# Optimization experiments

Measured on AMD Instinct MI355X. Metric: run time of the kernel, lower is better.

Reference implementation:

```python
import jax, jax.numpy as jnp
import numpy as np

B, T, IDIM, HDIM, K, LMAX, NLAYERS = 64, 1024, 120, 320, 72, 96, 3
LAMB = 0.1
NEG = -1e30


def lse3(a, b, c):
    m = jnp.maximum(jnp.maximum(a, b), c)
    return m + jnp.log(jnp.exp(a - m) + jnp.exp(b - m) + jnp.exp(c - m))


def _lstm_dir(x, Wih, Whh, bb):
    # x: [B,T,D] -> h: [B,T,H]; PyTorch gate order i,f,g,o
    gx = jnp.einsum('btd,gd->tbg', x, Wih) + bb  # [T,B,4H]
    def step(carry, g):
        h, c = carry
        g = g + h @ Whh.T
        i, f, gg, o = jnp.split(g, 4, axis=-1)
        c = jax.nn.sigmoid(f) * c + jax.nn.sigmoid(i) * jnp.tanh(gg)
        h = jax.nn.sigmoid(o) * jnp.tanh(c)
        return (h, c), h
    h0 = jnp.zeros((x.shape[0], HDIM), x.dtype)
    _, hs = jax.lax.scan(step, (h0, h0), gx)
    return hs.transpose(1, 0, 2)


def _rev(x, lengths):
    # reverse each sequence within its valid length (packed-sequence semantics)
    t = jnp.arange(x.shape[1])
    idx = jnp.where(t[None, :] < lengths[:, None], lengths[:, None] - 1 - t[None, :], t[None, :])
    return jnp.take_along_axis(x, idx[:, :, None], axis=1)


def _blstm_layer(x, Wih_f, Whh_f, b_f, Wih_b, Whh_b, b_b, lengths):
    hf = _lstm_dir(x, Wih_f, Whh_f, b_f)
    hb = _rev(_lstm_dir(_rev(x, lengths), Wih_b, Whh_b, b_b), lengths)
    return jnp.concatenate([hf, hb], axis=2)


def _ctc_forward(logp, labels, in_lens, lab_lens):
    # standard CTC alpha recursion (blank=0), log-space, vectorized over batch
    Bn, Tn, _ = logp.shape
    S = 2 * LMAX + 1
    ext = jnp.zeros((Bn, S), jnp.int32).at[:, 1::2].set(labels)  # blank-interleaved labels
    em = jnp.take_along_axis(logp, jnp.broadcast_to(ext[:, None, :], (Bn, Tn, S)), axis=2)
    em = em.transpose(1, 0, 2)  # [T,B,S]
    s_idx = jnp.arange(S)
    prev_lab = jnp.concatenate([jnp.full((Bn, 2), -1, jnp.int32), ext[:, :-2]], axis=1)
    can_skip = ((s_idx[None, :] % 2) == 1) & (ext != prev_lab)
    valid_s = s_idx[None, :] < (2 * lab_lens[:, None] + 1)
    alpha0 = jnp.full((Bn, S), NEG, logp.dtype)
    alpha0 = alpha0.at[:, 0].set(em[0][:, 0]).at[:, 1].set(em[0][:, 1])
    alpha0 = jnp.where(valid_s, alpha0, NEG)
    def step(alpha, inp):
        em_t, t = inp
        a2 = jnp.concatenate([jnp.full((Bn, 1), NEG, alpha.dtype), alpha[:, :-1]], axis=1)
        a3 = jnp.concatenate([jnp.full((Bn, 2), NEG, alpha.dtype), alpha[:, :-2]], axis=1)
        a3 = jnp.where(can_skip, a3, NEG)
        new = lse3(alpha, a2, a3) + em_t
        new = jnp.where(valid_s, new, NEG)
        new = jnp.where((t < in_lens)[:, None], new, alpha)  # freeze past utterance end
        return new, None
    alpha, _ = jax.lax.scan(step, alpha0, (em[1:], jnp.arange(1, Tn)))
    last = 2 * lab_lens
    aL = jnp.take_along_axis(alpha, last[:, None], axis=1)[:, 0]
    aLm1 = jnp.take_along_axis(alpha, (last - 1)[:, None], axis=1)[:, 0]
    return jnp.logaddexp(aL, aLm1)  # log p(labels | x)


def setup_inputs():
    key = jax.random.key(0)
    ks = jax.random.split(key, 12)
    H4 = 4 * HDIM
    s = 0.05
    return dict(
        logits=jax.random.normal(ks[0], (B, T, IDIM), jnp.float32),
        labels_padded=jax.random.randint(ks[1], (B, LMAX), 1, K).astype(jnp.int32),
        input_lengths=jax.random.randint(ks[2], (B,), T // 2, T + 1).astype(jnp.int32),
        label_lengths=jax.random.randint(ks[3], (B,), LMAX // 2, LMAX + 1).astype(jnp.int32),
        Wih0=jax.random.normal(ks[4], (2, H4, IDIM), jnp.float32) * s,
        Whh0=jax.random.normal(ks[5], (2, H4, HDIM), jnp.float32) * s,
        b0=jnp.zeros((2, H4), jnp.float32),
        Wih=jax.random.normal(ks[6], (NLAYERS - 1, 2, H4, 2 * HDIM), jnp.float32) * s,
        Whh=jax.random.normal(ks[7], (NLAYERS - 1, 2, H4, HDIM), jnp.float32) * s,
        b=jnp.zeros((NLAYERS - 1, 2, H4), jnp.float32),
        W_lin=jax.random.normal(ks[8], (K, 2 * HDIM), jnp.float32) * s,
        b_lin=jnp.zeros((K,), jnp.float32),
    )


def reference(logits, labels_padded, input_lengths, label_lengths, Wih0, Whh0, b0, Wih, Whh, b, W_lin, b_lin):
    # sort by input length descending (mirrors torch.sort + index_select)
    order = jnp.argsort(-input_lengths)
    logits = logits[order]
    labels_padded = labels_padded[order]
    input_lengths = input_lengths[order]
    label_lengths = label_lengths[order]
    # 3-layer BLSTM encoder
    x = _blstm_layer(logits, Wih0[0], Whh0[0], b0[0], Wih0[1], Whh0[1], b0[1], input_lengths)
    for l in range(NLAYERS - 1):
        x = _blstm_layer(x, Wih[l, 0], Whh[l, 0], b[l, 0], Wih[l, 1], Whh[l, 1], b[l, 1], input_lengths)
    netout = jax.nn.log_softmax(x @ W_lin.T + b_lin, axis=2)  # [B,T,K]
    # CTC-CRF: numerator = CTC alpha log-prob; denominator = free-running partition
    num = _ctc_forward(netout, labels_padded, input_lengths, label_lengths)
    tmask = jnp.arange(netout.shape[1])[None, :] < input_lengths[:, None]
    den = jnp.sum(jnp.where(tmask, jax.nn.logsumexp(netout, axis=2), 0.0), axis=1)
    return jnp.mean(den - (1.0 + LAMB) * num)
```

## Files before the change

### kernel.cpp

```cpp
#include <hip/hip_runtime.h>
#include <cstdint>
#include <cstddef>


typedef _Float16 f16;
typedef _Float16 h2v   __attribute__((ext_vector_type(2)));
typedef _Float16 f16x4v __attribute__((ext_vector_type(4)));
typedef _Float16 f16x8 __attribute__((ext_vector_type(8)));
typedef float    f32x4 __attribute__((ext_vector_type(4)));
typedef uint32_t u32x4 __attribute__((ext_vector_type(4)));

#define NEGF (-1e30f)
#define CT 128

__device__ __forceinline__ float dot2f(h2v a, h2v b, float c) {
#if __has_builtin(__builtin_amdgcn_fdot2)
  return __builtin_amdgcn_fdot2(a, b, c, false);
#else
  return c + (float)a.x * (float)b.x + (float)a.y * (float)b.y;
#endif
}

__device__ __forceinline__ float fast_rcp(float x) {
#if __has_builtin(__builtin_amdgcn_rcpf)
  return __builtin_amdgcn_rcpf(x);
#else
  return 1.f / x;
#endif
}
__device__ __forceinline__ float fsigm(float x) { return fast_rcp(1.f + __expf(-x)); }
__device__ __forceinline__ float ftanh(float x) { return 1.f - 2.f * fast_rcp(1.f + __expf(2.f * x)); }

__device__ __forceinline__ float fexp2(float x) {
#if __has_builtin(__builtin_amdgcn_exp2f)
  return __builtin_amdgcn_exp2f(x);
#else
  return exp2f(x);
#endif
}
__device__ __forceinline__ float flog2(float x) {
#if __has_builtin(__builtin_amdgcn_logf)
  return __builtin_amdgcn_logf(x);
#else
  return log2f(x);
#endif
}

__device__ __forceinline__ uint32_t poll_l2(const uint32_t* p) {
  uint32_t v;
  asm volatile("global_load_dword %0, %1, off sc0\n\t"
               "s_waitcnt vmcnt(0)"
               : "=&v"(v)
               : "v"(p)
               : "memory");
  return v;
}

__device__ __forceinline__ void stage16(f16* lds, const f16* g) {
#if __has_builtin(__builtin_amdgcn_global_load_lds)
  __builtin_amdgcn_global_load_lds(
      (const __attribute__((address_space(1))) uint32_t*)g,
      (__attribute__((address_space(3))) uint32_t*)lds, 16, 0, 0);
#else
  int lane = threadIdx.x & 63;
  *(f16x8*)&lds[lane * 8] = *(const f16x8*)g;
#endif
}


__global__ void conv_logits(const float* __restrict__ src, f16* __restrict__ dst) {
  int idx = blockIdx.x * 256 + threadIdx.x;
  int row = idx >> 7, k = idx & 127;
  dst[idx] = (f16)((k < 120) ? src[(size_t)row * 120 + k] : 0.f);
}

__global__ void conv_wt0(const float* __restrict__ w, f16* __restrict__ dst) {
  int idx = blockIdx.x * 256 + threadIdx.x;
  int n = idx >> 7, k = idx & 127;
  dst[idx] = (f16)((k < 120) ? w[(size_t)n * 120 + k] : 0.f);
}

__global__ void conv_copy(const float* __restrict__ src, f16* __restrict__ dst, int count) {
  int idx = blockIdx.x * 256 + threadIdx.x;
  if (idx < count) dst[idx] = (f16)src[idx];
}

__global__ void conv_wtl(const float* __restrict__ w, f16* __restrict__ dst) {
  int idx = blockIdx.x * 256 + threadIdx.x;
  int n = idx / 640, k = idx % 640;
  dst[idx] = (f16)((n < 72) ? w[(size_t)n * 640 + k] : 0.f);
}

__global__ void conv_whh(const float* __restrict__ whh0, const float* __restrict__ whh,
                         uint32_t* __restrict__ dst) {
  int o = blockIdx.x * 256 + threadIdx.x;
  int tid = o & 511;
  int g  = o >> 9;
  int j  = g % 40;
  int g2 = g / 40;
  int i  = g2 % 5;
  int g3 = g2 / 5;
  int hf = g3 & 1, slot = g3 >> 1;
  int tau = i * 512 + tid;
  int lr = tau >> 2, kq = tau & 3;
  int gate = lr / 160, u = lr - gate * 160;
  int r = gate * 320 + hf * 160 + u;
  int k = kq * 80 + j * 2;
  const float* srcm = (slot < 2) ? (whh0 + ((size_t)slot * 1280 + r) * 320)
                                 : (whh  + ((size_t)(slot - 2) * 1280 + r) * 320);
  f16 lo = (f16)srcm[k], hi = (f16)srcm[k + 1];
  dst[o] = (uint32_t)__builtin_bit_cast(unsigned short, lo) |
           ((uint32_t)__builtin_bit_cast(unsigned short, hi) << 16);
}

__global__ __launch_bounds__(256)
void gemm_chunk(const f16* __restrict__ A, const f16* __restrict__ W,
                f16* __restrict__ gxc, const int* __restrict__ lens,
                int lda, int kTiles, int c0) {
  __shared__ __align__(16) f16 As[128 * 32];
  __shared__ __align__(16) f16 Ws[2][128 * 32];
  const int tid = threadIdx.x;
  const int lane = tid & 63, wid = tid >> 6;
  const int wm = wid >> 1, wn = wid & 1;
  const int dir = blockIdx.y >> 6, b = blockIdx.y & 63;
  const int n0 = blockIdx.x * 256;
  const int r_base = lane >> 2;
  const int chs = ((((lane & 3) + (r_base >> 1)) & 3)) * 8;
  const int len = lens[b];

  f32x4 acc[4][8] = {};

  for (int kt = 0; kt < kTiles; ++kt) {
    const int k0 = kt * 32;
    __syncthreads();
#pragma unroll
    for (int hh = 0; hh < 2; ++hh) {
      const int c = wid * 2 + hh;
      const int j = c * 16 + r_base;
      const int s = c0 * CT + j;
      const int tt = dir ? ((s < len) ? (len - 1 - s) : s) : s;
      stage16(&As[c * 512], A + (size_t)(b * 1024 + tt) * lda + k0 + chs);
    }
#pragma unroll
    for (int hh = 0; hh < 4; ++hh) {
      const int c = wid * 4 + hh;
      const int tile = c >> 3, cc = c & 7;
      stage16(&Ws[tile][cc * 512],
              W + (size_t)(dir * 1280 + n0 + tile * 128 + cc * 16 + r_base) * lda + k0 + chs);
    }
    __syncthreads();

    const int q = lane >> 4;
    const int l15 = lane & 15;
    const int cs = (q - (l15 >> 1)) & 3;
    const int rofs = l15 * 32 + cs * 8;
    f16x8 av[4], wv0[4], wv1[4];
#pragma unroll
    for (int i = 0; i < 4; ++i)
      av[i] = *(const f16x8*)&As[(wm * 4 + i) * 512 + rofs];
#pragma unroll
    for (int i = 0; i < 4; ++i) {
      wv0[i] = *(const f16x8*)&Ws[0][(wn * 4 + i) * 512 + rofs];
      wv1[i] = *(const f16x8*)&Ws[1][(wn * 4 + i) * 512 + rofs];
    }
#pragma unroll
    for (int i = 0; i < 4; ++i)
#pragma unroll
      for (int j = 0; j < 4; ++j) {
        acc[i][j]     = __builtin_amdgcn_mfma_f32_16x16x32_f16(av[i], wv0[j], acc[i][j], 0, 0, 0);
        acc[i][4 + j] = __builtin_amdgcn_mfma_f32_16x16x32_f16(av[i], wv1[j], acc[i][4 + j], 0, 0, 0);
      }
  }

  const int r0 = (lane >> 4) * 4, cn = lane & 15;
  const size_t obase = (size_t)(dir * 64 + b) * CT;
#pragma unroll
  for (int i = 0; i < 4; ++i) {
    const int m = wm * 64 + i * 16 + r0;
#pragma unroll
    for (int j = 0; j < 4; ++j) {
      const int n = n0 + wn * 64 + j * 16 + cn;
#pragma unroll
      for (int r = 0; r < 4; ++r) {
        gxc[(obase + m + r) * 1280 + n]       = (f16)acc[i][j][r];
        gxc[(obase + m + r) * 1280 + n + 128] = (f16)acc[i][4 + j][r];
      }
    }
  }
}

__global__ void __launch_bounds__(512)
__attribute__((amdgpu_waves_per_eu(2, 2)))
lstm_scan_chunk(const volatile uint32_t* wbuf,
                const f16* __restrict__ gxc,
                const float* __restrict__ bias,
                const int* __restrict__ lens,
                f16* xnext,
                uint32_t* xq,
                uint32_t* xqf,
                f16* hsave,
                float* csave,
                int layer, int c0) {
  const int wg = blockIdx.x;
  const int half = wg >> 7;
  const int bd = wg & 127;
  const int b = bd >> 1, dir = bd & 1;
  const int tid = threadIdx.x;

  __shared__ __align__(16) f16 hbuf[320];
  __shared__ float ylds[640];
  __shared__ __align__(16) f16 hstage[64 * 160];

  h2v w[5][40];
  {
    const volatile uint32_t* wb =
        wbuf + (size_t)((layer * 2 + dir) * 2 + half) * 200 * 512;
#pragma unroll
    for (int i = 0; i < 5; ++i)
#pragma unroll
      for (int j = 0; j < 40; ++j) {
        uint32_t v = wb[(i * 40 + j) * 512 + tid];
        w[i][j] = __builtin_bit_cast(h2v, v);
      }
  }
  if (tid < 320) hbuf[tid] = (c0 == 0) ? (f16)0.f : hsave[bd * 320 + tid];

  const int len = lens[b];
  const int kq = tid & 3;
  const int qi = tid >> 2;
  const int gu = half * 160 + tid;
  float c_state = 0.f;
  float bi = 0.f, bff = 0.f, bg = 0.f, bo = 0.f;
  if (tid < 160) {
    if (c0 > 0) c_state = csave[wg * 160 + tid];
    const float* bp = bias + dir * 1280 + gu;
    bi = bp[0]; bff = bp[320]; bg = bp[640]; bo = bp[960];
  }
  __syncthreads();

  const size_t grow0 = (size_t)(dir * 64 + b) * CT;

  float gxi = 0.f, gxf = 0.f, gxg = 0.f, gxo = 0.f;
  if (tid < 160) {
    const f16* gp = gxc + grow0 * 1280 + gu;
    gxi = (float)gp[0]; gxf = (float)gp[320]; gxg = (float)gp[640]; gxo = (float)gp[960];
  }

  int fastmiss = 0;

  for (int tl = 0; tl < CT; ++tl) {
    const int s = c0 * CT + tl;
    const uint32_t tag = (uint32_t)(layer * 1024 + s + 1);

    float nxi = 0.f, nxf = 0.f, nxg = 0.f, nxo = 0.f;
    if (tid < 160 && tl + 1 < CT) {
      const f16* gp = gxc + (grow0 + tl + 1) * 1280 + gu;
      nxi = (float)gp[0]; nxf = (float)gp[320]; nxg = (float)gp[640]; nxo = (float)gp[960];
    }

    float a0 = 0.f, a1 = 0.f, a2 = 0.f, a3 = 0.f, a4 = 0.f;
    {
      const u32x4* h4 = (const u32x4*)hbuf;
#pragma unroll
      for (int jb = 0; jb < 5; ++jb) {
        u32x4 p = h4[kq * 10 + jb * 2];
        u32x4 q = h4[kq * 10 + jb * 2 + 1];
        h2v hr[8];
#pragma unroll
        for (int j = 0; j < 4; ++j) hr[j] = __builtin_bit_cast(h2v, p[j]);
#pragma unroll
        for (int j = 0; j < 4; ++j) hr[4 + j] = __builtin_bit_cast(h2v, q[j]);
#pragma unroll
        for (int j = 0; j < 8; ++j) {
          a0 = dot2f(w[0][jb * 8 + j], hr[j], a0);
          a1 = dot2f(w[1][jb * 8 + j], hr[j], a1);
          a2 = dot2f(w[2][jb * 8 + j], hr[j], a2);
          a3 = dot2f(w[3][jb * 8 + j], hr[j], a3);
          a4 = dot2f(w[4][jb * 8 + j], hr[j], a4);
        }
      }
    }
    {
      float av[5] = {a0, a1, a2, a3, a4};
#pragma unroll
      for (int i = 0; i < 5; ++i) {
        float v = av[i];
        v += __shfl_xor(v, 1, 64);
        v += __shfl_xor(v, 2, 64);
        if (kq == 0) ylds[i * 128 + qi] = v;
      }
    }

    if ((tl & 31) == 0 && tl > 0) {
      const int tw = tl - 32;
#pragma unroll
      for (int it = 0; it < 2; ++it) {
        const int slot = it * 512 + tid;
        if (slot < 640) {
          const int r = (int)(((unsigned)slot * 52429u) >> 20);
          const int j = slot - r * 20;
          const int sp = c0 * CT + tw + r;
          const int ttp = dir ? ((sp < len) ? (len - 1 - sp) : sp) : sp;
          f16x8 v = *(const f16x8*)&hstage[((tw + r) & 63) * 160 + j * 8];
          *(f16x8*)&xnext[(size_t)(b * 1024 + ttp) * 640 + dir * 320 + half * 160 + j * 8] = v;
        }
      }
    }
    __syncthreads();

    if (tid < 160) {
      const int u = tid;
      float pi = ylds[u]       + gxi + bi;
      float pf = ylds[160 + u] + gxf + bff;
      float pg = ylds[320 + u] + gxg + bg;
      float po = ylds[480 + u] + gxo + bo;
      float ig = fsigm(pi);
      float fg = fsigm(pf);
      float gg = ftanh(pg);
      float og = fsigm(po);
      c_state = fg * c_state + ig * gg;
      float hv = og * ftanh(c_state);
      const f16 hh = (f16)hv;
      const uint32_t word = (tag << 16) |
                            (uint32_t)__builtin_bit_cast(unsigned short, hh);
      const int qidx = ((bd * 2 + half) * 2 + (s & 1)) * 160 + u;
      __hip_atomic_store(&xqf[qidx], word, __ATOMIC_RELAXED,
                         __HIP_MEMORY_SCOPE_WORKGROUP);
      __hip_atomic_store(&xq[qidx], word, __ATOMIC_RELAXED,
                         __HIP_MEMORY_SCOPE_AGENT);
      hbuf[gu] = hh;
      hstage[(tl & 63) * 160 + u] = hh;
    } else if (tid >= 256 && tid < 416) {
      const int u = tid - 256;
      const int qidx = ((bd * 2 + (1 - half)) * 2 + (s & 1)) * 160 + u;
      uint32_t pw = 0;
      bool got = false;
      if (fastmiss < 2) {
        int tries = 16;
        do {
          pw = poll_l2(&xqf[qidx]);
        } while ((pw >> 16) != tag && --tries);
        got = ((pw >> 16) == tag);
        fastmiss = got ? 0 : (fastmiss + 1);
      }
      if (!got) {
        int spins = 0;
        do {
          pw = __hip_atomic_load(&xq[qidx], __ATOMIC_RELAXED,
                                 __HIP_MEMORY_SCOPE_AGENT);
        } while ((pw >> 16) != tag && ++spins < 200000);
      }
      hbuf[(1 - half) * 160 + u] =
          __builtin_bit_cast(f16, (unsigned short)(pw & 0xffffu));
    }
    __syncthreads();

    gxi = nxi; gxf = nxf; gxg = nxg; gxo = nxo;
  }

  {
    const int tw = CT - 32;
#pragma unroll
    for (int it = 0; it < 2; ++it) {
      const int slot = it * 512 + tid;
      if (slot < 640) {
        const int r = (int)(((unsigned)slot * 52429u) >> 20);
        const int j = slot - r * 20;
        const int sp = c0 * CT + tw + r;
        const int ttp = dir ? ((sp < len) ? (len - 1 - sp) : sp) : sp;
        f16x8 v = *(const f16x8*)&hstage[((tw + r) & 63) * 160 + j * 8];
        *(f16x8*)&xnext[(size_t)(b * 1024 + ttp) * 640 + dir * 320 + half * 160 + j * 8] = v;
      }
    }
  }
  if (tid < 160) {
    hsave[bd * 320 + gu] = hbuf[gu];
    csave[wg * 160 + tid] = c_state;
  }
}

__global__ __launch_bounds__(256)
void gemm_proj(const f16* __restrict__ A, const f16* __restrict__ W,
               float* __restrict__ outf, int lda, int kTiles, int ldo) {
  __shared__ __align__(16) f16 As[128 * 32];
  __shared__ __align__(16) f16 Ws[128 * 32];
  const int tid = threadIdx.x;
  const int lane = tid & 63, wid = tid >> 6;
  const int wm = wid >> 1, wn = wid & 1;
  const int m0 = blockIdx.y * 128, n0 = blockIdx.x * 128;
  const int r_base = lane >> 2;
  const int chs = ((((lane & 3) + (r_base >> 1)) & 3)) * 8;

  f32x4 acc[4][4] = {};

  for (int kt = 0; kt < kTiles; ++kt) {
    const int k0 = kt * 32;
    __syncthreads();
#pragma unroll
    for (int hh = 0; hh < 2; ++hh) {
      const int c = wid * 2 + hh;
      stage16(&As[c * 512], A + (size_t)(m0 + c * 16 + r_base) * lda + k0 + chs);
      stage16(&Ws[c * 512], W + (size_t)(n0 + c * 16 + r_base) * lda + k0 + chs);
    }
    __syncthreads();

    const int q = lane >> 4;
    const int l15 = lane & 15;
    const int cs = (q - (l15 >> 1)) & 3;
    const int rofs = l15 * 32 + cs * 8;
    f16x8 av[4], wv[4];
#pragma unroll
    for (int i = 0; i < 4; ++i)
      av[i] = *(const f16x8*)&As[(wm * 4 + i) * 512 + rofs];
#pragma unroll
    for (int i = 0; i < 4; ++i)
      wv[i] = *(const f16x8*)&Ws[(wn * 4 + i) * 512 + rofs];
#pragma unroll
    for (int i = 0; i < 4; ++i)
#pragma unroll
      for (int j = 0; j < 4; ++j)
        acc[i][j] = __builtin_amdgcn_mfma_f32_16x16x32_f16(av[i], wv[j], acc[i][j], 0, 0, 0);
  }

  const int r0 = (lane >> 4) * 4, cn = lane & 15;
#pragma unroll
  for (int i = 0; i < 4; ++i) {
    const int m = m0 + wm * 64 + i * 16 + r0;
#pragma unroll
    for (int j = 0; j < 4; ++j) {
      const int n = n0 + wn * 64 + j * 16 + cn;
#pragma unroll
      for (int r = 0; r < 4; ++r)
        outf[(size_t)(m + r) * ldo + n] = acc[i][j][r];
    }
  }
}

__global__ void lse_kernel(const float* __restrict__ Z, const float* __restrict__ b_lin,
                           float* __restrict__ lseout) {
  int row = blockIdx.x * 4 + (threadIdx.x >> 6);
  int l = threadIdx.x & 63;
  const float* z = Z + (size_t)row * 128;
  float v0 = (l < 72) ? z[l] + b_lin[l] : NEGF;
  float v1 = (l < 8) ? z[l + 64] + b_lin[l + 64] : NEGF;
  float m = fmaxf(v0, v1);
#pragma unroll
  for (int o = 32; o; o >>= 1) m = fmaxf(m, __shfl_xor(m, o, 64));
  float s = ((l < 72) ? __expf(v0 - m) : 0.f) + ((l < 8) ? __expf(v1 - m) : 0.f);
#pragma unroll
  for (int o = 32; o; o >>= 1) s += __shfl_xor(s, o, 64);
  if (l == 0) lseout[row] = m + __logf(s);
}

__global__ void emz_kernel(const float* __restrict__ Z, const float* __restrict__ lse,
                           const float* __restrict__ b_lin,
                           const int* __restrict__ labels,
                           f16* __restrict__ emc) {
  const int b = blockIdx.y;
  const int t0 = blockIdx.x * 4;
  const int tid = threadIdx.x;
  __shared__ int ext[200];
  __shared__ float bls[200];
  if (tid < 200) {
    int e = (tid < 193 && (tid & 1)) ? labels[b * 96 + (tid >> 1)] : 0;
    ext[tid] = e;
    bls[tid] = b_lin[e];
  }
  __syncthreads();
#pragma unroll
  for (int dt = 0; dt < 4; ++dt) {
    const int t = t0 + dt;
    const float lst = lse[b * 1024 + t];
    const float* zr = Z + ((size_t)(b * 1024 + t)) * 128;
    for (int s = tid; s < 200; s += 256)
      emc[((size_t)(b * 1024 + t)) * 200 + s] =
          (f16)((zr[ext[s]] + bls[s] - lst) * 1.4426950408889634f);
  }
}

__global__ void ctc_kernel(const f16* __restrict__ emc,
                           const int* __restrict__ labels, const int* __restrict__ inlen,
                           const int* __restrict__ lablen, float* __restrict__ num) {
  const int b = blockIdx.x;
  const int lane = threadIdx.x;
  __shared__ int ext[200];
  __shared__ float afin[200];

  for (int s = lane; s < 200; s += 64)
    ext[s] = (s < 193 && (s & 1)) ? labels[b * 96 + (s >> 1)] : 0;
  __syncthreads();

  const int L = lablen[b], len = inlen[b];
  const int Send = 2 * L + 1;
  const f16* eb = emc + (size_t)b * 1024 * 200;

  float a[4];
  bool  skp[4], val[4];
#pragma unroll
  for (int j = 0; j < 4; ++j) {
    const int s = lane * 4 + j;
    val[j] = (s < Send) && (s < 193);
    skp[j] = (s < 193) && (s & 1) && (s >= 2) && (ext[s] != ext[s - 2]);
  }
  {
    f16x4v e0 = *(const f16x4v*)&eb[lane * 4];
#pragma unroll
    for (int j = 0; j < 4; ++j) {
      const int s = lane * 4 + j;
      a[j] = (s <= 1 && val[j]) ? (float)e0[j] : NEGF;
    }
  }

  auto step = [&](f16x4v ev) {
    float p3 = __shfl_up(a[3], 1, 64);
    float p2 = __shfl_up(a[2], 1, 64);
    if (lane == 0) { p3 = NEGF; p2 = NEGF; }
    const float x2[4] = {p3, a[0], a[1], a[2]};
    const float x3[4] = {p2, p3, a[0], a[1]};
#pragma unroll
    for (int j = 0; j < 4; ++j) {
      const float xa = a[j], xb = x2[j];
      const float xc = skp[j] ? x3[j] : NEGF;
      const float m = fmaxf(xa, fmaxf(xb, xc));
      const float sum = fexp2(xa - m) + fexp2(xb - m) + fexp2(xc - m);
      const float nv = m + flog2(sum) + (float)ev[j];
      a[j] = val[j] ? nv : NEGF;
    }
  };

  f16x4v ring[8];
#pragma unroll
  for (int d = 1; d <= 8; ++d) {
    const int r = (d < len) ? d : (len - 1);
    ring[d & 7] = *(const f16x4v*)&eb[(size_t)r * 200 + lane * 4];
  }

  int t = 1;
  for (; t + 8 <= len; t += 8) {
#pragma unroll
    for (int k = 0; k < 8; ++k) {
      const int slot = (1 + k) & 7;
      f16x4v ev = ring[slot];
      const int tp = t + k + 8;
      if (tp < len)
        ring[slot] = *(const f16x4v*)&eb[(size_t)tp * 200 + lane * 4];
      step(ev);
    }
  }
  for (; t < len; ++t)
    step(*(const f16x4v*)&eb[(size_t)t * 200 + lane * 4]);

#pragma unroll
  for (int j = 0; j < 4; ++j) {
    const int s = lane * 4 + j;
    if (s < 193) afin[s] = a[j];
  }
  __syncthreads();
  if (lane == 0) {
    const float aL = afin[2 * L], aLm1 = afin[2 * L - 1];
    const float m = fmaxf(aL, aLm1);
    num[b] = 0.6931471805599453f * (m + flog2(fexp2(aL - m) + fexp2(aLm1 - m)));
  }
}

__global__ void final_kernel(const float* __restrict__ num, float* __restrict__ out) {
  int l = threadIdx.x;
  float v = -1.1f * num[l];
#pragma unroll
  for (int o = 32; o; o >>= 1) v += __shfl_xor(v, o, 64);
  if (l == 0) out[0] = v * (1.f / 64.f);
}

__global__ void sentinel_kernel(float* __restrict__ out, float code) { out[0] = code; }

extern "C" void kernel_launch(void* const* d_in, const int* in_sizes, int n_in,
                              void* d_out, int out_size, void* d_ws, size_t ws_size,
                              hipStream_t stream) {
  (void)in_sizes; (void)n_in; (void)out_size;

  const float* logits   = (const float*)d_in[0];
  const int*   labels   = (const int*)d_in[1];
  const int*   in_lens  = (const int*)d_in[2];
  const int*   lab_lens = (const int*)d_in[3];
  const float* Wih0     = (const float*)d_in[4];
  const float* Whh0     = (const float*)d_in[5];
  const float* b0       = (const float*)d_in[6];
  const float* Wih      = (const float*)d_in[7];
  const float* Whh      = (const float*)d_in[8];
  const float* bb       = (const float*)d_in[9];
  const float* W_lin    = (const float*)d_in[10];
  const float* b_lin    = (const float*)d_in[11];

  const size_t NEED = (size_t)224 * 1024 * 1024;
  if (ws_size < NEED) {
    sentinel_kernel<<<1, 1, 0, stream>>>((float*)d_out, -(float)(ws_size >> 20));
    return;
  }

  char* ws = (char*)d_ws;
  size_t off = 0;
  auto alloc = [&](size_t bytes) -> char* {
    char* p = ws + off;
    off += (bytes + 255) & ~(size_t)255;
    return p;
  };
  f16*      Xa     = (f16*)alloc((size_t)65536 * 640 * 2);
  f16*      Xb     = (f16*)alloc((size_t)65536 * 640 * 2);
  f16*      gxc    = (f16*)alloc((size_t)2 * 64 * CT * 1280 * 2);
  f16*      Wt0    = (f16*)alloc((size_t)2560 * 128 * 2);
  f16*      Wt12   = (f16*)alloc((size_t)2 * 2560 * 640 * 2);
  f16*      WtL    = (f16*)alloc((size_t)128 * 640 * 2);
  uint32_t* whh16  = (uint32_t*)alloc((size_t)6 * 2 * 200 * 512 * 4);
  float*    lseb   = (float*)alloc((size_t)65536 * 4);
  float*    num    = (float*)alloc(64 * 4);
  uint32_t* xq     = (uint32_t*)alloc((size_t)512 * 160 * 4);
  uint32_t* xqf    = (uint32_t*)alloc((size_t)512 * 160 * 4);
  f16*      hsave  = (f16*)alloc((size_t)128 * 320 * 2);
  float*    csave  = (float*)alloc((size_t)256 * 160 * 4);
  f16*      A0     = Xb;
  float*    Z      = (float*)gxc;
  f16*      emc    = Xa;

  hipMemsetAsync(xq, 0, (size_t)512 * 160 * 4, stream);
  hipMemsetAsync(xqf, 0, (size_t)512 * 160 * 4, stream);

  conv_logits<<<32768, 256, 0, stream>>>(logits, A0);
  conv_wt0<<<1280, 256, 0, stream>>>(Wih0, Wt0);
  conv_copy<<<12800, 256, 0, stream>>>(Wih, Wt12, 3276800);
  conv_wtl<<<320, 256, 0, stream>>>(W_lin, WtL);
  conv_whh<<<4800, 256, 0, stream>>>(Whh0, Whh, whh16);

  for (int c = 0; c < 1024 / CT; ++c) {
    gemm_chunk<<<dim3(5, 128), 256, 0, stream>>>(A0, Wt0, gxc, in_lens, 128, 4, c);
    lstm_scan_chunk<<<256, 512, 0, stream>>>(whh16, gxc, b0, in_lens, Xa, xq, xqf,
                                             hsave, csave, 0, c);
  }
  for (int c = 0; c < 1024 / CT; ++c) {
    gemm_chunk<<<dim3(5, 128), 256, 0, stream>>>(Xa, Wt12, gxc, in_lens, 640, 20, c);
    lstm_scan_chunk<<<256, 512, 0, stream>>>(whh16, gxc, bb, in_lens, Xb, xq, xqf,
                                             hsave, csave, 1, c);
  }
  for (int c = 0; c < 1024 / CT; ++c) {
    gemm_chunk<<<dim3(5, 128), 256, 0, stream>>>(Xb, Wt12 + (size_t)2560 * 640, gxc,
                                                 in_lens, 640, 20, c);
    lstm_scan_chunk<<<256, 512, 0, stream>>>(whh16, gxc, bb + 2560, in_lens, Xa, xq, xqf,
                                             hsave, csave, 2, c);
  }
  gemm_proj<<<dim3(1, 512), 256, 0, stream>>>(Xa, WtL, Z, 640, 20, 128);

  lse_kernel<<<16384, 256, 0, stream>>>(Z, b_lin, lseb);
  emz_kernel<<<dim3(256, 64), 256, 0, stream>>>(Z, lseb, b_lin, labels, emc);
  ctc_kernel<<<64, 64, 0, stream>>>(emc, labels, in_lens, lab_lens, num);
  final_kernel<<<1, 64, 0, stream>>>(num, (float*)d_out);
}
```

Before: 8.897 ms.

## Claim LSTM scan work slots per XCD so paired halves share an L2

Each LSTM scan workgroup now reads its hardware XCD id and atomically claims a slot from a per-XCD counter, falling back to other XCDs when one is full. The claimed slot decides which (batch, direction, half) the workgroup handles, so the two halves that exchange hidden state every step land on the same XCD and can communicate through the shared L2 instead of crossing dies. The fast-poll retry limits are also raised. In exchange, each launch pays for atomic counters and a per-launch counter region that must be zeroed, and the mapping depends on how the hardware distributes workgroups across XCDs.

```diff
diff --git a/kernel.cpp b/kernel.cpp
--- a/kernel.cpp
+++ b/kernel.cpp
@@ -200,12 +200,33 @@
                 uint32_t* xqf,
                 f16* hsave,
                 float* csave,
+                int* cnt,
                 int layer, int c0) {
-  const int wg = blockIdx.x;
-  const int half = wg >> 7;
-  const int bd = wg & 127;
+  const int tid = threadIdx.x;
+
+  __shared__ int s_claim;
+  if (tid == 0) {
+    uint32_t xcd;
+    asm volatile("s_getreg_b32 %0, hwreg(HW_REG_XCC_ID)" : "=s"(xcd));
+    xcd &= 7;
+    int slot = __hip_atomic_fetch_add(&cnt[xcd], 1, __ATOMIC_RELAXED,
+                                      __HIP_MEMORY_SCOPE_AGENT);
+    if (slot >= 32) {
+      for (int d = 1;; d = (d == 7) ? 1 : d + 1) {
+        int x2 = (xcd + d) & 7;
+        slot = __hip_atomic_fetch_add(&cnt[x2], 1, __ATOMIC_RELAXED,
+                                      __HIP_MEMORY_SCOPE_AGENT);
+        if (slot < 32) { xcd = (uint32_t)x2; break; }
+      }
+    }
+    s_claim = (int)(xcd * 32) + slot;
+  }
+  __syncthreads();
+  const int claim = s_claim;
+  const int bd = claim >> 1;
+  const int half = claim & 1;
   const int b = bd >> 1, dir = bd & 1;
-  const int tid = threadIdx.x;
+  const int wgq = half * 128 + bd;
 
   __shared__ __align__(16) f16 hbuf[320];
   __shared__ float ylds[640];
@@ -232,7 +253,7 @@
   float c_state = 0.f;
   float bi = 0.f, bff = 0.f, bg = 0.f, bo = 0.f;
   if (tid < 160) {
-    if (c0 > 0) c_state = csave[wg * 160 + tid];
+    if (c0 > 0) c_state = csave[wgq * 160 + tid];
     const float* bp = bias + dir * 1280 + gu;
     bi = bp[0]; bff = bp[320]; bg = bp[640]; bo = bp[960];
   }
@@ -335,8 +356,8 @@
       const int qidx = ((bd * 2 + (1 - half)) * 2 + (s & 1)) * 160 + u;
       uint32_t pw = 0;
       bool got = false;
-      if (fastmiss < 2) {
-        int tries = 16;
+      if (fastmiss < 3) {
+        int tries = 24;
         do {
           pw = poll_l2(&xqf[qidx]);
         } while ((pw >> 16) != tag && --tries);
@@ -375,7 +396,7 @@
   }
   if (tid < 160) {
     hsave[bd * 320 + gu] = hbuf[gu];
-    csave[wg * 160 + tid] = c_state;
+    csave[wgq * 160 + tid] = c_state;
   }
 }
 
@@ -617,12 +638,14 @@
   uint32_t* xqf    = (uint32_t*)alloc((size_t)512 * 160 * 4);
   f16*      hsave  = (f16*)alloc((size_t)128 * 320 * 2);
   float*    csave  = (float*)alloc((size_t)256 * 160 * 4);
+  int*      xcdcnt = (int*)alloc((size_t)24 * 16 * 4);
   f16*      A0     = Xb;
   float*    Z      = (float*)gxc;
   f16*      emc    = Xa;
 
   hipMemsetAsync(xq, 0, (size_t)512 * 160 * 4, stream);
   hipMemsetAsync(xqf, 0, (size_t)512 * 160 * 4, stream);
+  hipMemsetAsync(xcdcnt, 0, (size_t)24 * 16 * 4, stream);
 
   conv_logits<<<32768, 256, 0, stream>>>(logits, A0);
   conv_wt0<<<1280, 256, 0, stream>>>(Wih0, Wt0);
@@ -633,18 +656,21 @@
   for (int c = 0; c < 1024 / CT; ++c) {
     gemm_chunk<<<dim3(5, 128), 256, 0, stream>>>(A0, Wt0, gxc, in_lens, 128, 4, c);
     lstm_scan_chunk<<<256, 512, 0, stream>>>(whh16, gxc, b0, in_lens, Xa, xq, xqf,
-                                             hsave, csave, 0, c);
+                                             hsave, csave, xcdcnt + (0 * 8 + c) * 16,
+                                             0, c);
   }
   for (int c = 0; c < 1024 / CT; ++c) {
     gemm_chunk<<<dim3(5, 128), 256, 0, stream>>>(Xa, Wt12, gxc, in_lens, 640, 20, c);
     lstm_scan_chunk<<<256, 512, 0, stream>>>(whh16, gxc, bb, in_lens, Xb, xq, xqf,
-                                             hsave, csave, 1, c);
+                                             hsave, csave, xcdcnt + (1 * 8 + c) * 16,
+                                             1, c);
   }
   for (int c = 0; c < 1024 / CT; ++c) {
     gemm_chunk<<<dim3(5, 128), 256, 0, stream>>>(Xb, Wt12 + (size_t)2560 * 640, gxc,
                                                  in_lens, 640, 20, c);
     lstm_scan_chunk<<<256, 512, 0, stream>>>(whh16, gxc, bb + 2560, in_lens, Xa, xq, xqf,
-                                             hsave, csave, 2, c);
+                                             hsave, csave, xcdcnt + (2 * 8 + c) * 16,
+                                             2, c);
   }
   gemm_proj<<<dim3(1, 512), 256, 0, stream>>>(Xa, WtL, Z, 640, 20, 128);
 
```

Measured after the change: 9.032 ms. About the same (+1.5%).

## Interleave two sequences per LSTM workgroup to hide cross-workgroup h exchange latency

Applied to the files above, without the earlier changes.

Each scan workgroup now handles two batch sequences (b and b+32) with the same weights, alternating phases. While it computes one sequence's matvec, the partner workgroup's half of the other sequence's hidden state is in flight, so the cross-WG polling latency overlaps with compute. Grid halves from 256 to 128 workgroups. The workgroup-scope fast poll path (xqf) is removed. The trade-off is fewer active CUs and roughly double serial work per workgroup per timestep.

```diff
diff --git a/kernel.cpp b/kernel.cpp
--- a/kernel.cpp
+++ b/kernel.cpp
@@ -44,16 +44,6 @@
 #else
   return log2f(x);
 #endif
-}
-
-__device__ __forceinline__ uint32_t poll_l2(const uint32_t* p) {
-  uint32_t v;
-  asm volatile("global_load_dword %0, %1, off sc0\n\t"
-               "s_waitcnt vmcnt(0)"
-               : "=&v"(v)
-               : "v"(p)
-               : "memory");
-  return v;
 }
 
 __device__ __forceinline__ void stage16(f16* lds, const f16* g) {
@@ -197,19 +187,23 @@
                 const int* __restrict__ lens,
                 f16* xnext,
                 uint32_t* xq,
-                uint32_t* xqf,
                 f16* hsave,
                 float* csave,
                 int layer, int c0) {
+  const int tid = threadIdx.x;
   const int wg = blockIdx.x;
-  const int half = wg >> 7;
-  const int bd = wg & 127;
-  const int b = bd >> 1, dir = bd & 1;
-  const int tid = threadIdx.x;
-
-  __shared__ __align__(16) f16 hbuf[320];
+  const int half = wg & 1;
+  const int pi = wg >> 1;
+  const int dir = pi & 1;
+  const int bA = pi >> 1;
+  const int bB = bA + 32;
+  const int bdA = bA * 2 + dir, bdB = bB * 2 + dir;
+
+  __shared__ __align__(16) f16 hbufA[320];
+  __shared__ __align__(16) f16 hbufB[320];
   __shared__ float ylds[640];
-  __shared__ __align__(16) f16 hstage[64 * 160];
+  __shared__ __align__(16) f16 hstA[64 * 160];
+  __shared__ __align__(16) f16 hstB[64 * 160];
 
   h2v w[5][40];
   {
@@ -223,143 +217,62 @@
         w[i][j] = __builtin_bit_cast(h2v, v);
       }
   }
-  if (tid < 320) hbuf[tid] = (c0 == 0) ? (f16)0.f : hsave[bd * 320 + tid];
-
-  const int len = lens[b];
+  if (tid < 320) {
+    hbufA[tid] = (c0 == 0) ? (f16)0.f : hsave[bdA * 320 + tid];
+    hbufB[tid] = (c0 == 0) ? (f16)0.f : hsave[bdB * 320 + tid];
+  }
+
+  const int lenA = lens[bA], lenB = lens[bB];
   const int kq = tid & 3;
   const int qi = tid >> 2;
   const int gu = half * 160 + tid;
-  float c_state = 0.f;
+  float cA = 0.f, cB = 0.f;
   float bi = 0.f, bff = 0.f, bg = 0.f, bo = 0.f;
   if (tid < 160) {
-    if (c0 > 0) c_state = csave[wg * 160 + tid];
+    if (c0 > 0) {
+      cA = csave[(half * 128 + bdA) * 160 + tid];
+      cB = csave[(half * 128 + bdB) * 160 + tid];
+    }
     const float* bp = bias + dir * 1280 + gu;
     bi = bp[0]; bff = bp[320]; bg = bp[640]; bo = bp[960];
   }
   __syncthreads();
 
-  const size_t grow0 = (size_t)(dir * 64 + b) * CT;
-
-  float gxi = 0.f, gxf = 0.f, gxg = 0.f, gxo = 0.f;
-  if (tid < 160) {
-    const f16* gp = gxc + grow0 * 1280 + gu;
-    gxi = (float)gp[0]; gxf = (float)gp[320]; gxg = (float)gp[640]; gxo = (float)gp[960];
-  }
-
-  int fastmiss = 0;
-
-  for (int tl = 0; tl < CT; ++tl) {
-    const int s = c0 * CT + tl;
-    const uint32_t tag = (uint32_t)(layer * 1024 + s + 1);
-
-    float nxi = 0.f, nxf = 0.f, nxg = 0.f, nxo = 0.f;
-    if (tid < 160 && tl + 1 < CT) {
-      const f16* gp = gxc + (grow0 + tl + 1) * 1280 + gu;
-      nxi = (float)gp[0]; nxf = (float)gp[320]; nxg = (float)gp[640]; nxo = (float)gp[960];
-    }
-
+  const size_t growA = (size_t)(dir * 64 + bA) * CT;
+  const size_t growB = (size_t)(dir * 64 + bB) * CT;
+
+  auto dophase = [&](const f16* hb) {
     float a0 = 0.f, a1 = 0.f, a2 = 0.f, a3 = 0.f, a4 = 0.f;
-    {
-      const u32x4* h4 = (const u32x4*)hbuf;
-#pragma unroll
-      for (int jb = 0; jb < 5; ++jb) {
-        u32x4 p = h4[kq * 10 + jb * 2];
-        u32x4 q = h4[kq * 10 + jb * 2 + 1];
-        h2v hr[8];
-#pragma unroll
-        for (int j = 0; j < 4; ++j) hr[j] = __builtin_bit_cast(h2v, p[j]);
-#pragma unroll
-        for (int j = 0; j < 4; ++j) hr[4 + j] = __builtin_bit_cast(h2v, q[j]);
-#pragma unroll
-        for (int j = 0; j < 8; ++j) {
-          a0 = dot2f(w[0][jb * 8 + j], hr[j], a0);
-          a1 = dot2f(w[1][jb * 8 + j], hr[j], a1);
-          a2 = dot2f(w[2][jb * 8 + j], hr[j], a2);
-          a3 = dot2f(w[3][jb * 8 + j], hr[j], a3);
-          a4 = dot2f(w[4][jb * 8 + j], hr[j], a4);
-        }
+    const u32x4* h4 = (const u32x4*)hb;
+#pragma unroll
+    for (int jb = 0; jb < 5; ++jb) {
+      u32x4 p = h4[kq * 10 + jb * 2];
+      u32x4 q = h4[kq * 10 + jb * 2 + 1];
+      h2v hr[8];
+#pragma unroll
+      for (int j = 0; j < 4; ++j) hr[j] = __builtin_bit_cast(h2v, p[j]);
+#pragma unroll
+      for (int j = 0; j < 4; ++j) hr[4 + j] = __builtin_bit_cast(h2v, q[j]);
+#pragma unroll
+      for (int j = 0; j < 8; ++j) {
+        a0 = dot2f(w[0][jb * 8 + j], hr[j], a0);
+        a1 = dot2f(w[1][jb * 8 + j], hr[j], a1);
+        a2 = dot2f(w[2][jb * 8 + j], hr[j], a2);
+        a3 = dot2f(w[3][jb * 8 + j], hr[j], a3);
+        a4 = dot2f(w[4][jb * 8 + j], hr[j], a4);
       }
     }
-    {
-      float av[5] = {a0, a1, a2, a3, a4};
-#pragma unroll
-      for (int i = 0; i < 5; ++i) {
-        float v = av[i];
-        v += __shfl_xor(v, 1, 64);
-        v += __shfl_xor(v, 2, 64);
-        if (kq == 0) ylds[i * 128 + qi] = v;
-      }
-    }
-
-    if ((tl & 31) == 0 && tl > 0) {
-      const int tw = tl - 32;
-#pragma unroll
-      for (int it = 0; it < 2; ++it) {
-        const int slot = it * 512 + tid;
-        if (slot < 640) {
-          const int r = (int)(((unsigned)slot * 52429u) >> 20);
-          const int j = slot - r * 20;
-          const int sp = c0 * CT + tw + r;
-          const int ttp = dir ? ((sp < len) ? (len - 1 - sp) : sp) : sp;
-          f16x8 v = *(const f16x8*)&hstage[((tw + r) & 63) * 160 + j * 8];
-          *(f16x8*)&xnext[(size_t)(b * 1024 + ttp) * 640 + dir * 320 + half * 160 + j * 8] = v;
-        }
-      }
-    }
-    __syncthreads();
-
-    if (tid < 160) {
-      const int u = tid;
-      float pi = ylds[u]       + gxi + bi;
-      float pf = ylds[160 + u] + gxf + bff;
-      float pg = ylds[320 + u] + gxg + bg;
-      float po = ylds[480 + u] + gxo + bo;
-      float ig = fsigm(pi);
-      float fg = fsigm(pf);
-      float gg = ftanh(pg);
-      float og = fsigm(po);
-      c_state = fg * c_state + ig * gg;
-      float hv = og * ftanh(c_state);
-      const f16 hh = (f16)hv;
-      const uint32_t word = (tag << 16) |
-                            (uint32_t)__builtin_bit_cast(unsigned short, hh);
-      const int qidx = ((bd * 2 + half) * 2 + (s & 1)) * 160 + u;
-      __hip_atomic_store(&xqf[qidx], word, __ATOMIC_RELAXED,
-                         __HIP_MEMORY_SCOPE_WORKGROUP);
-      __hip_atomic_store(&xq[qidx], word, __ATOMIC_RELAXED,
-                         __HIP_MEMORY_SCOPE_AGENT);
-      hbuf[gu] = hh;
-      hstage[(tl & 63) * 160 + u] = hh;
-    } else if (tid >= 256 && tid < 416) {
-      const int u = tid - 256;
-      const int qidx = ((bd * 2 + (1 - half)) * 2 + (s & 1)) * 160 + u;
-      uint32_t pw = 0;
-      bool got = false;
-      if (fastmiss < 2) {
-        int tries = 16;
-        do {
-          pw = poll_l2(&xqf[qidx]);
-        } while ((pw >> 16) != tag && --tries);
-        got = ((pw >> 16) == tag);
-        fastmiss = got ? 0 : (fastmiss + 1);
-      }
-      if (!got) {
-        int spins = 0;
-        do {
-          pw = __hip_atomic_load(&xq[qidx], __ATOMIC_RELAXED,
-                                 __HIP_MEMORY_SCOPE_AGENT);
-        } while ((pw >> 16) != tag && ++spins < 200000);
-      }
-      hbuf[(1 - half) * 160 + u] =
-          __builtin_bit_cast(f16, (unsigned short)(pw & 0xffffu));
-    }
-    __syncthreads();
-
-    gxi = nxi; gxf = nxf; gxg = nxg; gxo = nxo;
-  }
-
-  {
-    const int tw = CT - 32;
+    float av[5] = {a0, a1, a2, a3, a4};
+#pragma unroll
+    for (int i = 0; i < 5; ++i) {
+      float v = av[i];
+      v += __shfl_xor(v, 1, 64);
+      v += __shfl_xor(v, 2, 64);
+      if (kq == 0) ylds[i * 128 + qi] = v;
+    }
+  };
+
+  auto flush = [&](int tw, const f16* hst, int bX, int lenX) {
 #pragma unroll
     for (int it = 0; it < 2; ++it) {
       const int slot = it * 512 + tid;
@@ -367,15 +280,107 @@
         const int r = (int)(((unsigned)slot * 52429u) >> 20);
         const int j = slot - r * 20;
         const int sp = c0 * CT + tw + r;
-        const int ttp = dir ? ((sp < len) ? (len - 1 - sp) : sp) : sp;
-        f16x8 v = *(const f16x8*)&hstage[((tw + r) & 63) * 160 + j * 8];
-        *(f16x8*)&xnext[(size_t)(b * 1024 + ttp) * 640 + dir * 320 + half * 160 + j * 8] = v;
+        const int ttp = dir ? ((sp < lenX) ? (lenX - 1 - sp) : sp) : sp;
+        f16x8 v = *(const f16x8*)&hst[((tw + r) & 63) * 160 + j * 8];
+        *(f16x8*)&xnext[(size_t)(bX * 1024 + ttp) * 640 + dir * 320 + half * 160 + j * 8] = v;
       }
     }
-  }
+  };
+
+  for (int tl = 0; tl < CT; ++tl) {
+    const int s = c0 * CT + tl;
+
+    float gxiA = 0.f, gxfA = 0.f, gxgA = 0.f, gxoA = 0.f;
+    float gxiB = 0.f, gxfB = 0.f, gxgB = 0.f, gxoB = 0.f;
+    if (tid < 160) {
+      const f16* gA = gxc + (growA + tl) * 1280 + gu;
+      gxiA = (float)gA[0]; gxfA = (float)gA[320]; gxgA = (float)gA[640]; gxoA = (float)gA[960];
+      const f16* gB = gxc + (growB + tl) * 1280 + gu;
+      gxiB = (float)gB[0]; gxfB = (float)gB[320]; gxgB = (float)gB[640]; gxoB = (float)gB[960];
+    }
+
+    dophase(hbufA);
+    if ((tl & 31) == 0 && tl > 0) {
+      flush(tl - 32, hstA, bA, lenA);
+      flush(tl - 32, hstB, bB, lenB);
+    }
+    __syncthreads();
+
+    if (tid < 160) {
+      const int u = tid;
+      float pi_ = ylds[u]       + gxiA + bi;
+      float pf_ = ylds[160 + u] + gxfA + bff;
+      float pg_ = ylds[320 + u] + gxgA + bg;
+      float po_ = ylds[480 + u] + gxoA + bo;
+      float ig = fsigm(pi_), fg = fsigm(pf_), gg = ftanh(pg_), og = fsigm(po_);
+      cA = fg * cA + ig * gg;
+      float hv = og * ftanh(cA);
+      const f16 hh = (f16)hv;
+      const uint32_t tagA = (uint32_t)(layer * 1024 + s + 1);
+      const uint32_t word = (tagA << 16) |
+                            (uint32_t)__builtin_bit_cast(unsigned short, hh);
+      __hip_atomic_store(&xq[((bdA * 2 + half) * 2 + (s & 1)) * 160 + u], word,
+                         __ATOMIC_RELAXED, __HIP_MEMORY_SCOPE_AGENT);
+      hbufA[gu] = hh;
+      hstA[(tl & 63) * 160 + u] = hh;
+    } else if (tid >= 256 && tid < 416 && tl > 0) {
+      const int u = tid - 256;
+      const uint32_t tagB = (uint32_t)(layer * 1024 + s);
+      const int qidx = ((bdB * 2 + (1 - half)) * 2 + ((s - 1) & 1)) * 160 + u;
+      uint32_t pw;
+      int spins = 0;
+      do {
+        pw = __hip_atomic_load(&xq[qidx], __ATOMIC_RELAXED,
+                               __HIP_MEMORY_SCOPE_AGENT);
+      } while ((pw >> 16) != tagB && ++spins < 200000);
+      hbufB[(1 - half) * 160 + u] =
+          __builtin_bit_cast(f16, (unsigned short)(pw & 0xffffu));
+    }
+    __syncthreads();
+
+    dophase(hbufB);
+    __syncthreads();
+
+    if (tid < 160) {
+      const int u = tid;
+      float pi_ = ylds[u]       + gxiB + bi;
+      float pf_ = ylds[160 + u] + gxfB + bff;
+      float pg_ = ylds[320 + u] + gxgB + bg;
+      float po_ = ylds[480 + u] + gxoB + bo;
+      float ig = fsigm(pi_), fg = fsigm(pf_), gg = ftanh(pg_), og = fsigm(po_);
+      cB = fg * cB + ig * gg;
+      float hv = og * ftanh(cB);
+      const f16 hh = (f16)hv;
+      const uint32_t tagB1 = (uint32_t)(layer * 1024 + s + 1);
+      const uint32_t word = (tagB1 << 16) |
+                            (uint32_t)__builtin_bit_cast(unsigned short, hh);
+      __hip_atomic_store(&xq[((bdB * 2 + half) * 2 + (s & 1)) * 160 + u], word,
+                         __ATOMIC_RELAXED, __HIP_MEMORY_SCOPE_AGENT);
+      hbufB[gu] = hh;
+      hstB[(tl & 63) * 160 + u] = hh;
+    } else if (tid >= 256 && tid < 416 && tl + 1 < CT) {
+      const int u = tid - 256;
+      const uint32_t tagA1 = (uint32_t)(layer * 1024 + s + 1);
+      const int qidx = ((bdA * 2 + (1 - half)) * 2 + (s & 1)) * 160 + u;
+      uint32_t pw;
+      int spins = 0;
+      do {
+        pw = __hip_atomic_load(&xq[qidx], __ATOMIC_RELAXED,
+                               __HIP_MEMORY_SCOPE_AGENT);
+      } while ((pw >> 16) != tagA1 && ++spins < 200000);
+      hbufA[(1 - half) * 160 + u] =
+          __builtin_bit_cast(f16, (unsigned short)(pw & 0xffffu));
+    }
+    __syncthreads();
+  }
+
+  flush(CT - 32, hstA, bA, lenA);
+  flush(CT - 32, hstB, bB, lenB);
   if (tid < 160) {
-    hsave[bd * 320 + gu] = hbuf[gu];
-    csave[wg * 160 + tid] = c_state;
+    hsave[bdA * 320 + gu] = hbufA[gu];
+    hsave[bdB * 320 + gu] = hbufB[gu];
+    csave[(half * 128 + bdA) * 160 + tid] = cA;
+    csave[(half * 128 + bdB) * 160 + tid] = cB;
   }
 }
 
@@ -614,7 +619,6 @@
   float*    lseb   = (float*)alloc((size_t)65536 * 4);
   float*    num    = (float*)alloc(64 * 4);
   uint32_t* xq     = (uint32_t*)alloc((size_t)512 * 160 * 4);
-  uint32_t* xqf    = (uint32_t*)alloc((size_t)512 * 160 * 4);
   f16*      hsave  = (f16*)alloc((size_t)128 * 320 * 2);
   float*    csave  = (float*)alloc((size_t)256 * 160 * 4);
   f16*      A0     = Xb;
@@ -622,7 +626,6 @@
   f16*      emc    = Xa;
 
   hipMemsetAsync(xq, 0, (size_t)512 * 160 * 4, stream);
-  hipMemsetAsync(xqf, 0, (size_t)512 * 160 * 4, stream);
 
   conv_logits<<<32768, 256, 0, stream>>>(logits, A0);
   conv_wt0<<<1280, 256, 0, stream>>>(Wih0, Wt0);
@@ -632,18 +635,18 @@
 
   for (int c = 0; c < 1024 / CT; ++c) {
     gemm_chunk<<<dim3(5, 128), 256, 0, stream>>>(A0, Wt0, gxc, in_lens, 128, 4, c);
-    lstm_scan_chunk<<<256, 512, 0, stream>>>(whh16, gxc, b0, in_lens, Xa, xq, xqf,
+    lstm_scan_chunk<<<128, 512, 0, stream>>>(whh16, gxc, b0, in_lens, Xa, xq,
                                              hsave, csave, 0, c);
   }
   for (int c = 0; c < 1024 / CT; ++c) {
     gemm_chunk<<<dim3(5, 128), 256, 0, stream>>>(Xa, Wt12, gxc, in_lens, 640, 20, c);
-    lstm_scan_chunk<<<256, 512, 0, stream>>>(whh16, gxc, bb, in_lens, Xb, xq, xqf,
+    lstm_scan_chunk<<<128, 512, 0, stream>>>(whh16, gxc, bb, in_lens, Xb, xq,
                                              hsave, csave, 1, c);
   }
   for (int c = 0; c < 1024 / CT; ++c) {
     gemm_chunk<<<dim3(5, 128), 256, 0, stream>>>(Xb, Wt12 + (size_t)2560 * 640, gxc,
                                                  in_lens, 640, 20, c);
-    lstm_scan_chunk<<<256, 512, 0, stream>>>(whh16, gxc, bb + 2560, in_lens, Xa, xq, xqf,
+    lstm_scan_chunk<<<128, 512, 0, stream>>>(whh16, gxc, bb + 2560, in_lens, Xa, xq,
                                              hsave, csave, 2, c);
   }
   gemm_proj<<<dim3(1, 512), 256, 0, stream>>>(Xa, WtL, Z, 640, 20, 128);
```

After: 13.01 ms. +46.2%, slower.
